# Optimization experiments

Measured on AMD Instinct MI355X. Metric: run time of the kernel, lower is better.

## Reference

```python
import jax, jax.numpy as jnp
import numpy as np

NH = 12
LEVEL = 4  # Lmin = 2**LEVEL = 16


def _build_sets(T, Lmin):
    l_list, r_list = [], []
    L = Lmin
    while L <= T:
        for i in range(T // L):
            l_list.append(i * L)
            r_list.append((i + 1) * L - 1)
        L *= 2
    return np.asarray(l_list, np.int32), np.asarray(r_list, np.int32)


def _get_slice(x_cum, l_idx, r_idx):
    # x_cum: [B,nh,T,hs]; returns inclusive range-sums x[l..r] via cumsum diffs
    r = x_cum[:, :, r_idx, :]
    l = x_cum[:, :, np.maximum(np.asarray(l_idx) - 1, 0), :]
    mask = (np.asarray(l_idx) >= 1).astype(x_cum.dtype)[None, None, :, None]
    return r - l * mask


def _get_slice_dyn(x_cum, l_idx, r_idx):
    # same but with traced/jnp indices (tail term)
    r = x_cum[:, :, r_idx, :]
    l = x_cum[:, :, jnp.maximum(l_idx - 1, 0), :]
    mask = (l_idx >= 1).astype(x_cum.dtype)[None, None, :, None]
    return r - l * mask


def setup_inputs() -> dict:
    key = jax.random.key(0)
    k0, k1, k2, k3 = jax.random.split(key, 4)
    B, T, C = 8, 2048, 768
    hs = C // NH
    s = 0.02
    return {
        "x": jax.random.normal(k0, (B, T, C), jnp.float32),
        "Wqkv": jax.random.normal(k1, (3 * C, C), jnp.float32) * s,
        "Wproj": jax.random.normal(k2, (C, C), jnp.float32) * s,
        "Wv": jax.random.normal(k3, (hs, hs * hs), jnp.float32) * s,
        "bv": jnp.zeros((hs,), jnp.float32),
    }


def reference(x, Wqkv, Wproj, Wv, bv):
    B, T, C = x.shape
    nh = NH
    hs = C // nh
    Lmin = 2 ** LEVEL
    scale = 1.0 / jnp.sqrt(jnp.asarray(hs, x.dtype))

    qkv = x @ Wqkv.T  # [B,T,3C]
    q, k, v0 = jnp.split(qkv, 3, axis=-1)
    q = q.reshape(B, T, nh, hs).transpose(0, 2, 1, 3)   # [B,nh,T,hs]
    k = k.reshape(B, T, nh, hs).transpose(0, 2, 1, 3)
    v0 = v0.reshape(B, T, nh, hs).transpose(0, 2, 1, 3)

    # v = v_proj(outer(k, v0).flatten)  == einsum with Wv reshaped [hs,hs,hs]
    Wv3 = Wv.reshape(hs, hs, hs)
    v = jnp.einsum('bhti,bhtj,eij->bhte', k, v0, Wv3) + bv

    k_cum = jnp.cumsum(k, axis=2)
    v_cum = jnp.cumsum(v, axis=2)

    l_idx, r_idx = _build_sets(T, Lmin)  # static dyadic sets
    K = _get_slice(k_cum, l_idx, r_idx)  # [B,nh,S,hs]
    V = _get_slice(v_cum, l_idx, r_idx)

    t_idx = jnp.arange(T)
    mask = t_idx[:, None] >= jnp.asarray(r_idx)[None, :]  # [T,S]
    logits = jnp.einsum('bhtd,bhsd->bhts', q, K) * scale
    logits = jnp.where(mask[None, None], logits, -jnp.inf)

    # tail: remainder within the current Lmin block
    l_tail = (t_idx // Lmin) * Lmin
    K_tail = _get_slice_dyn(k_cum, l_tail, t_idx)  # [B,nh,T,hs]
    V_tail = _get_slice_dyn(v_cum, l_tail, t_idx)
    tail_logits = jnp.sum(q * K_tail, axis=-1) * scale  # [B,nh,T]

    att = jax.nn.softmax(jnp.concatenate([logits, tail_logits[..., None]], axis=-1), axis=-1)
    out = jnp.einsum('bhts,bhsd->bhtd', att[..., :-1], V) + att[..., -1:] * V_tail
    out = out.transpose(0, 2, 1, 3).reshape(B, T, C)
    return out @ Wproj.T
```

## Files before the change

### kernel.cpp

```cpp
#include <hip/hip_runtime.h>


typedef float  f32x4  __attribute__((ext_vector_type(4)));
typedef _Float16 half8 __attribute__((ext_vector_type(8)));
typedef _Float16 half4 __attribute__((ext_vector_type(4)));

#define DEV __device__ __forceinline__
#define MFMA16(a, b, c) __builtin_amdgcn_mfma_f32_16x16x32_f16((a), (b), (c), 0, 0, 0)
#define GLOAD16(gp, lp)                                                  \
  __builtin_amdgcn_global_load_lds(                                      \
      (const __attribute__((address_space(1))) unsigned int*)(gp),       \
      (__attribute__((address_space(3))) unsigned int*)(lp), 16, 0, 0)

__global__ __launch_bounds__(256) void k_cast16(const float* __restrict__ in,
                                                _Float16* __restrict__ outh, int n4) {
  int i = blockIdx.x * 256 + threadIdx.x;
  if (i >= n4) return;
  f32x4 v = ((const f32x4*)in)[i];
  half4 o;
#pragma unroll
  for (int c = 0; c < 4; ++c) o[c] = (_Float16)v[c];
  ((half4*)outh)[i] = o;
}

__global__ __launch_bounds__(256, 3) void k_gemm_qkv(
    const _Float16* __restrict__ A16, const _Float16* __restrict__ B16,
    _Float16* __restrict__ qo, _Float16* __restrict__ ko, _Float16* __restrict__ v0o) {
  __shared__ _Float16 sA[128][64], sB[128][64];
  const int K = 768;
  int tid = threadIdx.x, lane = tid & 63, wave = tid >> 6;
  int l15 = lane & 15, g = lane >> 4;
  int wr = wave >> 1, wc = wave & 1;
  int n0 = blockIdx.x * 128, m0 = blockIdx.y * 128;
  f32x4 acc[4][4];
#pragma unroll
  for (int a = 0; a < 4; ++a)
#pragma unroll
    for (int b = 0; b < 4; ++b) acc[a][b] = f32x4{0.f, 0.f, 0.f, 0.f};
  int rsel = lane >> 3;
  int csel = (lane & 7) ^ rsel;
  for (int k0 = 0; k0 < K; k0 += 64) {
#pragma unroll
    for (int r = 0; r < 4; ++r) {
      int row = wave * 32 + r * 8 + rsel;
      GLOAD16(&A16[(size_t)(m0 + row) * K + k0 + csel * 8], &sA[wave * 32 + r * 8][0]);
      GLOAD16(&B16[(size_t)(n0 + row) * K + k0 + csel * 8], &sB[wave * 32 + r * 8][0]);
    }
    __syncthreads();
#pragma unroll
    for (int kk = 0; kk < 2; ++kk) {
      int kc = kk * 4 + g;
      int cc = ((kc ^ (l15 & 7)) << 3);
      half8 af[4], bf[4];
#pragma unroll
      for (int mf = 0; mf < 4; ++mf) af[mf] = *(const half8*)&sA[wr * 64 + mf * 16 + l15][cc];
#pragma unroll
      for (int nf = 0; nf < 4; ++nf) bf[nf] = *(const half8*)&sB[wc * 64 + nf * 16 + l15][cc];
#pragma unroll
      for (int mf = 0; mf < 4; ++mf)
#pragma unroll
        for (int nf = 0; nf < 4; ++nf)
          acc[mf][nf] = MFMA16(af[mf], bf[nf], acc[mf][nf]);
    }
    __syncthreads();
  }
  int sec = n0 / 768;
  int nb = n0 - sec * 768;
#pragma unroll
  for (int mf = 0; mf < 4; ++mf)
#pragma unroll
    for (int nf = 0; nf < 4; ++nf)
#pragma unroll
      for (int r = 0; r < 4; ++r) {
        int m = m0 + wr * 64 + mf * 16 + (g << 2) + r;
        int n = nb + wc * 64 + nf * 16 + l15;
        int b = m >> 11, t = m & 2047;
        int h = n >> 6, d = n & 63;
        size_t idx = (((size_t)b * 12 + h) * 2048 + t) * 64 + d;
        _Float16 val = (_Float16)acc[mf][nf][r];
        if (sec == 0) qo[idx] = val;
        else if (sec == 1) ko[idx] = val;
        else v0o[idx] = val;
      }
}

__global__ __launch_bounds__(256, 3) void k_veins(
    const _Float16* __restrict__ kh, const _Float16* __restrict__ v0g,
    const _Float16* __restrict__ Wvh, const float* __restrict__ bv,
    _Float16* __restrict__ vout) {
  __shared__ _Float16 ks[256][72];
  __shared__ _Float16 sB[2][64][64];
  int tid = threadIdx.x, lane = tid & 63, wave = tid >> 6;
  int l15 = lane & 15, g = lane >> 4, g8 = g << 3;
  size_t row0 = (size_t)blockIdx.x * 256;

  int srow_lo = wave * 8 + (lane >> 3);
  int scsrc = (lane & 7) ^ (lane >> 3);
  auto STAGE = [&](int b, int i) {
#pragma unroll
    for (int h = 0; h < 2; ++h) {
      GLOAD16(&Wvh[(size_t)(h * 32 + srow_lo) * 4096 + i * 64 + (scsrc << 3)],
              ((_Float16*)sB) + (size_t)b * 4096 + (h * 256 + wave * 64) * 8);
    }
  };

#pragma unroll
  for (int r = 0; r < 8; ++r) {
    int row = (tid >> 3) + r * 32;
    int c8 = (tid & 7) << 3;
    *(half8*)&ks[row][c8] = *(const half8*)&kh[(row0 + row) * 64 + c8];
  }
  half8 v0r[4][2];
#pragma unroll
  for (int mf = 0; mf < 4; ++mf) {
    size_t rb = (row0 + wave * 64 + mf * 16 + l15) * 64;
#pragma unroll
    for (int kk = 0; kk < 2; ++kk)
      v0r[mf][kk] = *(const half8*)&v0g[rb + kk * 32 + g8];
  }
  f32x4 acc[4][4];
#pragma unroll
  for (int a = 0; a < 4; ++a)
#pragma unroll
    for (int b = 0; b < 4; ++b) acc[a][b] = f32x4{0.f, 0.f, 0.f, 0.f};

  STAGE(0, 0);
  __syncthreads();
  int r0 = wave * 64 + l15;
  for (int i8 = 0; i8 < 8; ++i8) {
    half8 kr0 = *(const half8*)&ks[r0][i8 * 8];
    half8 kr1 = *(const half8*)&ks[r0 + 16][i8 * 8];
    half8 kr2 = *(const half8*)&ks[r0 + 32][i8 * 8];
    half8 kr3 = *(const half8*)&ks[r0 + 48][i8 * 8];
#pragma unroll
    for (int ii = 0; ii < 8; ++ii) {
      int i = i8 * 8 + ii;
      int cur = i & 1;
      if (i < 63) STAGE(cur ^ 1, i + 1);
      half8 b0[4], b1[4];
#pragma unroll
      for (int nf = 0; nf < 4; ++nf) {
        b0[nf] = *(const half8*)&sB[cur][nf * 16 + l15][((g ^ (l15 & 7)) << 3)];
        b1[nf] = *(const half8*)&sB[cur][nf * 16 + l15][(((4 + g) ^ (l15 & 7)) << 3)];
      }
      _Float16 kv0 = kr0[ii], kv1 = kr1[ii], kv2 = kr2[ii], kv3 = kr3[ii];
      {
        half8 a0 = v0r[0][0] * kv0, a1 = v0r[1][0] * kv1;
        half8 a2 = v0r[2][0] * kv2, a3 = v0r[3][0] * kv3;
#pragma unroll
        for (int nf = 0; nf < 4; ++nf) {
          acc[0][nf] = MFMA16(a0, b0[nf], acc[0][nf]);
          acc[1][nf] = MFMA16(a1, b0[nf], acc[1][nf]);
          acc[2][nf] = MFMA16(a2, b0[nf], acc[2][nf]);
          acc[3][nf] = MFMA16(a3, b0[nf], acc[3][nf]);
        }
      }
      {
        half8 a0 = v0r[0][1] * kv0, a1 = v0r[1][1] * kv1;
        half8 a2 = v0r[2][1] * kv2, a3 = v0r[3][1] * kv3;
#pragma unroll
        for (int nf = 0; nf < 4; ++nf) {
          acc[0][nf] = MFMA16(a0, b1[nf], acc[0][nf]);
          acc[1][nf] = MFMA16(a1, b1[nf], acc[1][nf]);
          acc[2][nf] = MFMA16(a2, b1[nf], acc[2][nf]);
          acc[3][nf] = MFMA16(a3, b1[nf], acc[3][nf]);
        }
      }
      __syncthreads();
    }
  }
#pragma unroll
  for (int mf = 0; mf < 4; ++mf)
#pragma unroll
    for (int nf = 0; nf < 4; ++nf) {
      int e = (nf << 4) + l15;
      float bve = bv[e];
#pragma unroll
      for (int r = 0; r < 4; ++r) {
        int row = wave * 64 + mf * 16 + (g << 2) + r;
        vout[(row0 + row) * 64 + e] = (_Float16)(acc[mf][nf][r] + bve);
      }
    }
}

__global__ __launch_bounds__(256) void k_segments(
    const _Float16* __restrict__ kmat, const _Float16* __restrict__ vmat,
    _Float16* __restrict__ Ks, _Float16* __restrict__ Vt) {
  __shared__ float Ls[255][64];
  int bh = blockIdx.x, tid = threadIdx.x;
  size_t bh2048 = (size_t)bh * 2048;
  for (int task = tid; task < 8192; task += 256) {
    int seg = task >> 6, d = task & 63;
    const _Float16* p = kmat + (bh2048 + seg * 16) * 64 + d;
    float s = 0.f;
#pragma unroll
    for (int u = 0; u < 16; ++u) s += (float)p[u * 64];
    Ls[seg][d] = s;
  }
  __syncthreads();
  {
    int bprev = 0, bcur = 128, cnt = 64;
    for (int lev = 1; lev < 8; ++lev) {
      for (int task = tid; task < cnt * 64; task += 256) {
        int i = task >> 6, d = task & 63;
        Ls[bcur + i][d] = Ls[bprev + 2 * i][d] + Ls[bprev + 2 * i + 1][d];
      }
      __syncthreads();
      bprev = bcur; bcur += cnt; cnt >>= 1;
    }
  }
  for (int task = tid; task < 16384; task += 256) {
    int seg = task >> 6;
    float v = (seg < 255) ? Ls[seg][task & 63] : 0.f;
    Ks[(size_t)bh * 16384 + task] = (_Float16)v;
  }
  __syncthreads();
  for (int task = tid; task < 8192; task += 256) {
    int seg = task >> 6, d = task & 63;
    const _Float16* p = vmat + (bh2048 + seg * 16) * 64 + d;
    float s = 0.f;
#pragma unroll
    for (int u = 0; u < 16; ++u) s += (float)p[u * 64];
    Ls[seg][d] = s;
  }
  __syncthreads();
  {
    int bprev = 0, bcur = 128, cnt = 64;
    for (int lev = 1; lev < 8; ++lev) {
      for (int task = tid; task < cnt * 64; task += 256) {
        int i = task >> 6, d = task & 63;
        Ls[bcur + i][d] = Ls[bprev + 2 * i][d] + Ls[bprev + 2 * i + 1][d];
      }
      __syncthreads();
      bprev = bcur; bcur += cnt; cnt >>= 1;
    }
  }
  for (int task = tid; task < 16384; task += 256) {
    int d = task >> 8, seg = task & 255;
    float v = (seg < 255) ? Ls[seg][d] : 0.f;
    Vt[(size_t)bh * 16384 + task] = (_Float16)v;
  }
}

__global__ __launch_bounds__(256) void k_attn2(
    const _Float16* __restrict__ qm, const _Float16* __restrict__ km,
    const _Float16* __restrict__ vm,
    const _Float16* __restrict__ Ks, const _Float16* __restrict__ Vt,
    _Float16* __restrict__ outp) {
  __shared__ __align__(16) _Float16 P[4][16][296];
  __shared__ __align__(16) _Float16 tK[4][16][72];
  __shared__ __align__(16) _Float16 tV[4][16][72];
  int tid = threadIdx.x, lane = tid & 63, wave = tid >> 6;
  int orig = blockIdx.y * 32 + blockIdx.x;
  int wg = (orig & 7) * 384 + (orig >> 3);
  int tile = wg & 31, bh = wg >> 5;
  int t0 = tile * 64, tw0 = t0 + wave * 16;
  size_t bh2048 = (size_t)bh * 2048;
  int l15 = lane & 15, g = lane >> 4, g8 = g << 3;

  {
    const _Float16* kp = km + (bh2048 + tw0) * 64 + lane;
    const _Float16* vp = vm + (bh2048 + tw0) * 64 + lane;
    float ka = 0.f, va = 0.f;
#pragma unroll
    for (int t = 0; t < 16; ++t) {
      ka += (float)kp[t * 64];
      va += (float)vp[t * 64];
      tK[wave][t][lane] = (_Float16)ka;
      tV[wave][t][lane] = (_Float16)va;
    }
  }
  half8 qf[2];
  {
    const _Float16* qp = qm + (bh2048 + tw0 + l15) * 64 + g8;
    qf[0] = *(const half8*)qp;
    qf[1] = *(const half8*)(qp + 32);
  }
  unsigned mA = 0, mE = 0;
#pragma unroll
  for (int nf = 0; nf < 16; ++nf) {
    int seg = nf * 16 + l15;
    if (seg < 255) {
      int m = 256 - seg;
      int cl = 32 - __clz(m - 1);
      int lev = 8 - cl;
      int rdx = (seg - (256 - (256 >> lev)) + 1) * (16 << lev) - 1;
      if (rdx < tw0) mA |= 1u << nf;
      else if (rdx == tw0 + 15) mE |= 1u << nf;
    }
  }
  unsigned mAny = mA | mE;
  unsigned pmask = 0;
#pragma unroll
  for (int ks = 0; ks < 8; ++ks)
    if (__any((int)((mAny >> (2 * ks)) & 3u))) pmask |= 1u << ks;

  f32x4 acc[17];
#pragma unroll
  for (int i = 0; i < 17; ++i) acc[i] = f32x4{0.f, 0.f, 0.f, 0.f};
  const _Float16* KsB = Ks + (size_t)bh * 16384;
#pragma unroll
  for (int ks = 0; ks < 8; ++ks) {
    if ((pmask >> ks) & 1) {
      const _Float16* ph = KsB + (size_t)(ks * 32 + l15) * 64 + g8;
      half8 h00 = *(const half8*)ph;
      half8 h01 = *(const half8*)(ph + 32);
      half8 h10 = *(const half8*)(ph + 1024);
      half8 h11 = *(const half8*)(ph + 1056);
      acc[2 * ks] = MFMA16(qf[0], h00, acc[2 * ks]);
      acc[2 * ks] = MFMA16(qf[1], h01, acc[2 * ks]);
      acc[2 * ks + 1] = MFMA16(qf[0], h10, acc[2 * ks + 1]);
      acc[2 * ks + 1] = MFMA16(qf[1], h11, acc[2 * ks + 1]);
    }
  }
  {
    const _Float16* tp = &tK[wave][l15][g8];
    half8 t0f = *(const half8*)tp;
    half8 t1f = *(const half8*)(tp + 32);
    acc[16] = MFMA16(qf[0], t0f, acc[16]);
    acc[16] = MFMA16(qf[1], t1f, acc[16]);
  }

  const float scale = 0.125f;
  float mx[4], sm[4], et[4];
#pragma unroll
  for (int r = 0; r < 4; ++r) {
    int tr = g * 4 + r;
    mx[r] = (l15 == tr) ? acc[16][r] * scale : -3.0e38f;
  }
#pragma unroll
  for (int nf = 0; nf < 16; ++nf) {
    bool bA = (mA >> nf) & 1, bE = (mE >> nf) & 1;
#pragma unroll
    for (int r = 0; r < 4; ++r) {
      bool u = bA || (bE && g == 3 && r == 3);
      if (u) mx[r] = fmaxf(mx[r], acc[nf][r] * scale);
    }
  }
#pragma unroll
  for (int off = 1; off < 16; off <<= 1)
#pragma unroll
    for (int r = 0; r < 4; ++r) mx[r] = fmaxf(mx[r], __shfl_xor(mx[r], off));
#pragma unroll
  for (int r = 0; r < 4; ++r) {
    int tr = g * 4 + r;
    et[r] = (l15 == tr) ? __expf(acc[16][r] * scale - mx[r]) : 0.f;
    sm[r] = et[r];
  }
#pragma unroll
  for (int ks = 0; ks < 8; ++ks) {
    if ((pmask >> ks) & 1) {
#pragma unroll
      for (int f = 0; f < 2; ++f) {
        int nf = 2 * ks + f;
        bool bA = (mA >> nf) & 1, bE = (mE >> nf) & 1;
#pragma unroll
        for (int r = 0; r < 4; ++r) {
          bool u = bA || (bE && g == 3 && r == 3);
          float e = u ? __expf(acc[nf][r] * scale - mx[r]) : 0.f;
          acc[nf][r] = e;
          sm[r] += e;
        }
      }
    }
  }
#pragma unroll
  for (int off = 1; off < 16; off <<= 1)
#pragma unroll
    for (int r = 0; r < 4; ++r) sm[r] += __shfl_xor(sm[r], off);
  float inv[4];
#pragma unroll
  for (int r = 0; r < 4; ++r) inv[r] = 1.f / sm[r];

  half8 zz = {};
  *(half8*)&P[wave][lane >> 2][256 + (lane & 3) * 8] = zz;
#pragma unroll
  for (int nf = 0; nf < 16; ++nf)
#pragma unroll
    for (int r = 0; r < 4; ++r)
      P[wave][g * 4 + r][nf * 16 + l15] = (_Float16)(acc[nf][r] * inv[r]);
#pragma unroll
  for (int r = 0; r < 4; ++r)
    if (l15 == g * 4 + r) P[wave][l15][256 + l15] = (_Float16)(et[r] * inv[r]);

  f32x4 oa[4];
#pragma unroll
  for (int i = 0; i < 4; ++i) oa[i] = f32x4{0.f, 0.f, 0.f, 0.f};
  const _Float16* VB = Vt + (size_t)bh * 16384;
#pragma unroll
  for (int ks = 0; ks < 8; ++ks) {
    if ((pmask >> ks) & 1) {
      half8 pa = *(const half8*)&P[wave][l15][ks * 32 + g8];
#pragma unroll
      for (int n2 = 0; n2 < 4; ++n2) {
        half8 vb = *(const half8*)(VB + (size_t)(n2 * 16 + l15) * 256 + ks * 32 + g8);
        oa[n2] = MFMA16(pa, vb, oa[n2]);
      }
    }
  }
  {
    half8 pa = *(const half8*)&P[wave][l15][256 + g8];
    int jb = (g & 1) * 8;
#pragma unroll
    for (int n2 = 0; n2 < 4; ++n2) {
      half8 vt;
#pragma unroll
      for (int jj = 0; jj < 8; ++jj) vt[jj] = tV[wave][jb + jj][n2 * 16 + l15];
      oa[n2] = MFMA16(pa, vt, oa[n2]);
    }
  }
  int b = bh / 12, h = bh - b * 12;
  size_t obase = ((size_t)b * 2048 + tw0) * 768 + h * 64;
#pragma unroll
  for (int n2 = 0; n2 < 4; ++n2)
#pragma unroll
    for (int r = 0; r < 4; ++r)
      outp[obase + (size_t)(g * 4 + r) * 768 + n2 * 16 + l15] = (_Float16)oa[n2][r];
}

__global__ __launch_bounds__(256, 3) void k_gemm_proj(
    const _Float16* __restrict__ A16, const _Float16* __restrict__ B16,
    float* __restrict__ C) {
  __shared__ _Float16 sA[128][64], sB[128][64];
  const int K = 768;
  int tid = threadIdx.x, lane = tid & 63, wave = tid >> 6;
  int l15 = lane & 15, g = lane >> 4;
  int wr = wave >> 1, wc = wave & 1;
  int n0 = blockIdx.x * 128, m0 = blockIdx.y * 128;
  f32x4 acc[4][4];
#pragma unroll
  for (int a = 0; a < 4; ++a)
#pragma unroll
    for (int b = 0; b < 4; ++b) acc[a][b] = f32x4{0.f, 0.f, 0.f, 0.f};
  int rsel = lane >> 3;
  int csel = (lane & 7) ^ rsel;
  for (int k0 = 0; k0 < K; k0 += 64) {
#pragma unroll
    for (int r = 0; r < 4; ++r) {
      int row = wave * 32 + r * 8 + rsel;
      GLOAD16(&A16[(size_t)(m0 + row) * K + k0 + csel * 8], &sA[wave * 32 + r * 8][0]);
      GLOAD16(&B16[(size_t)(n0 + row) * K + k0 + csel * 8], &sB[wave * 32 + r * 8][0]);
    }
    __syncthreads();
#pragma unroll
    for (int kk = 0; kk < 2; ++kk) {
      int kc = kk * 4 + g;
      int cc = ((kc ^ (l15 & 7)) << 3);
      half8 af[4], bf[4];
#pragma unroll
      for (int mf = 0; mf < 4; ++mf) af[mf] = *(const half8*)&sA[wr * 64 + mf * 16 + l15][cc];
#pragma unroll
      for (int nf = 0; nf < 4; ++nf) bf[nf] = *(const half8*)&sB[wc * 64 + nf * 16 + l15][cc];
#pragma unroll
      for (int mf = 0; mf < 4; ++mf)
#pragma unroll
        for (int nf = 0; nf < 4; ++nf)
          acc[mf][nf] = MFMA16(af[mf], bf[nf], acc[mf][nf]);
    }
    __syncthreads();
  }
#pragma unroll
  for (int mf = 0; mf < 4; ++mf)
#pragma unroll
    for (int nf = 0; nf < 4; ++nf)
#pragma unroll
      for (int r = 0; r < 4; ++r) {
        int m = m0 + wr * 64 + mf * 16 + (g << 2) + r;
        int n = n0 + wc * 64 + nf * 16 + l15;
        C[(size_t)m * 768 + n] = acc[mf][nf][r];
      }
}

extern "C" void kernel_launch(void* const* d_in, const int* in_sizes, int n_in,
                              void* d_out, int out_size, void* d_ws, size_t ws_size,
                              hipStream_t stream) {
  const float* x = (const float*)d_in[0];
  const float* Wqkv = (const float*)d_in[1];
  const float* Wproj = (const float*)d_in[2];
  const float* Wv = (const float*)d_in[3];
  const float* bv = (const float*)d_in[4];
  float* out = (float*)d_out;
  char* ws = (char*)d_ws;
  size_t off = 0;
  auto alloc = [&](size_t bytes) -> void* {
    void* p = (void*)(ws + off);
    off += (bytes + 255) & ~(size_t)255;
    return p;
  };
  _Float16* x16  = (_Float16*)alloc(12582912ull * 2);
  _Float16* wq16 = (_Float16*)alloc(1769472ull * 2);
  _Float16* wv16 = (_Float16*)alloc(262144ull * 2 + 8192);
  _Float16* wp16 = (_Float16*)alloc(589824ull * 2);
  _Float16* q16  = (_Float16*)alloc(12582912ull * 2);
  _Float16* k16  = (_Float16*)alloc(12582912ull * 2);
  _Float16* v016 = (_Float16*)alloc(12582912ull * 2);
  _Float16* vm16 = (_Float16*)alloc(12582912ull * 2);
  _Float16* Ks   = (_Float16*)alloc(1572864ull * 2);
  _Float16* Vt   = (_Float16*)alloc(1572864ull * 2);
  _Float16* outp = (_Float16*)alloc(12582912ull * 2);

  k_cast16<<<dim3(12288), dim3(256), 0, stream>>>(x, x16, 3145728);
  k_cast16<<<dim3(1728), dim3(256), 0, stream>>>(Wqkv, wq16, 442368);
  k_cast16<<<dim3(256), dim3(256), 0, stream>>>(Wv, wv16, 65536);
  k_cast16<<<dim3(576), dim3(256), 0, stream>>>(Wproj, wp16, 147456);
  k_gemm_qkv<<<dim3(18, 128), dim3(256), 0, stream>>>(x16, wq16, q16, k16, v016);
  k_veins<<<dim3(768), dim3(256), 0, stream>>>(k16, v016, wv16, bv, vm16);
  k_segments<<<dim3(96), dim3(256), 0, stream>>>(k16, vm16, Ks, Vt);
  k_attn2<<<dim3(32, 96), dim3(256), 0, stream>>>(q16, k16, vm16, Ks, Vt, outp);
  k_gemm_proj<<<dim3(6, 128), dim3(256), 0, stream>>>(outp, wp16, out);
}
```

Baseline: 356.2 us.

## Remap GEMM workgroups per XCD, use exp2 softmax, shrink P tile, add setprio

The QKV and projection GEMMs now launch as flat 1D grids and remap block ids so that consecutive tiles land on the same XCD, aiming for better L2 reuse of the weight and activation panels. In the attention kernel the softmax folds log2(e) into the scale and uses exp2f, and the P buffer is narrowed now that the tail block only needs 16 columns. The tail V fragment is zero-filled for the unused lane groups. s_setprio brackets the MFMA phases so waves issuing matrix work get scheduling priority. Each piece is small, and together they touch several kernels with separate tuning intents.

```diff
diff --git a/kernel.cpp b/kernel.cpp
--- a/kernel.cpp
+++ b/kernel.cpp
@@ -31,7 +31,8 @@
   int tid = threadIdx.x, lane = tid & 63, wave = tid >> 6;
   int l15 = lane & 15, g = lane >> 4;
   int wr = wave >> 1, wc = wave & 1;
-  int n0 = blockIdx.x * 128, m0 = blockIdx.y * 128;
+  int wg = (blockIdx.x & 7) * 288 + (blockIdx.x >> 3);
+  int n0 = (wg % 18) * 128, m0 = (wg / 18) * 128;
   f32x4 acc[4][4];
 #pragma unroll
   for (int a = 0; a < 4; ++a)
@@ -247,7 +248,7 @@
     const _Float16* __restrict__ vm,
     const _Float16* __restrict__ Ks, const _Float16* __restrict__ Vt,
     _Float16* __restrict__ outp) {
-  __shared__ __align__(16) _Float16 P[4][16][296];
+  __shared__ __align__(16) _Float16 P[4][16][280];
   __shared__ __align__(16) _Float16 tK[4][16][72];
   __shared__ __align__(16) _Float16 tV[4][16][72];
   int tid = threadIdx.x, lane = tid & 63, wave = tid >> 6;
@@ -299,6 +300,7 @@
 #pragma unroll
   for (int i = 0; i < 17; ++i) acc[i] = f32x4{0.f, 0.f, 0.f, 0.f};
   const _Float16* KsB = Ks + (size_t)bh * 16384;
+  __builtin_amdgcn_s_setprio(1);
 #pragma unroll
   for (int ks = 0; ks < 8; ++ks) {
     if ((pmask >> ks) & 1) {
@@ -320,13 +322,14 @@
     acc[16] = MFMA16(qf[0], t0f, acc[16]);
     acc[16] = MFMA16(qf[1], t1f, acc[16]);
   }
-
-  const float scale = 0.125f;
+  __builtin_amdgcn_s_setprio(0);
+
+  const float c = 0.125f * 1.44269504f;
   float mx[4], sm[4], et[4];
 #pragma unroll
   for (int r = 0; r < 4; ++r) {
     int tr = g * 4 + r;
-    mx[r] = (l15 == tr) ? acc[16][r] * scale : -3.0e38f;
+    mx[r] = (l15 == tr) ? acc[16][r] * c : -3.0e38f;
   }
 #pragma unroll
   for (int nf = 0; nf < 16; ++nf) {
@@ -334,7 +337,7 @@
 #pragma unroll
     for (int r = 0; r < 4; ++r) {
       bool u = bA || (bE && g == 3 && r == 3);
-      if (u) mx[r] = fmaxf(mx[r], acc[nf][r] * scale);
+      if (u) mx[r] = fmaxf(mx[r], acc[nf][r] * c);
     }
   }
 #pragma unroll
@@ -344,7 +347,7 @@
 #pragma unroll
   for (int r = 0; r < 4; ++r) {
     int tr = g * 4 + r;
-    et[r] = (l15 == tr) ? __expf(acc[16][r] * scale - mx[r]) : 0.f;
+    et[r] = (l15 == tr) ? exp2f(acc[16][r] * c - mx[r]) : 0.f;
     sm[r] = et[r];
   }
 #pragma unroll
@@ -357,7 +360,7 @@
 #pragma unroll
         for (int r = 0; r < 4; ++r) {
           bool u = bA || (bE && g == 3 && r == 3);
-          float e = u ? __expf(acc[nf][r] * scale - mx[r]) : 0.f;
+          float e = u ? exp2f(acc[nf][r] * c - mx[r]) : 0.f;
           acc[nf][r] = e;
           sm[r] += e;
         }
@@ -372,8 +375,10 @@
 #pragma unroll
   for (int r = 0; r < 4; ++r) inv[r] = 1.f / sm[r];
 
-  half8 zz = {};
-  *(half8*)&P[wave][lane >> 2][256 + (lane & 3) * 8] = zz;
+  {
+    half4 z4 = {};
+    *(half4*)&P[wave][lane >> 2][256 + (lane & 3) * 4] = z4;
+  }
 #pragma unroll
   for (int nf = 0; nf < 16; ++nf)
 #pragma unroll
@@ -387,6 +392,7 @@
 #pragma unroll
   for (int i = 0; i < 4; ++i) oa[i] = f32x4{0.f, 0.f, 0.f, 0.f};
   const _Float16* VB = Vt + (size_t)bh * 16384;
+  __builtin_amdgcn_s_setprio(1);
 #pragma unroll
   for (int ks = 0; ks < 8; ++ks) {
     if ((pmask >> ks) & 1) {
@@ -399,16 +405,18 @@
     }
   }
   {
-    half8 pa = *(const half8*)&P[wave][l15][256 + g8];
-    int jb = (g & 1) * 8;
+    half8 pa = *(const half8*)&P[wave][l15][256 + (g & 1) * 8];
 #pragma unroll
     for (int n2 = 0; n2 < 4; ++n2) {
-      half8 vt;
-#pragma unroll
-      for (int jj = 0; jj < 8; ++jj) vt[jj] = tV[wave][jb + jj][n2 * 16 + l15];
+      half8 vt = {};
+      if (g < 2) {
+#pragma unroll
+        for (int jj = 0; jj < 8; ++jj) vt[jj] = tV[wave][g8 + jj][n2 * 16 + l15];
+      }
       oa[n2] = MFMA16(pa, vt, oa[n2]);
     }
   }
+  __builtin_amdgcn_s_setprio(0);
   int b = bh / 12, h = bh - b * 12;
   size_t obase = ((size_t)b * 2048 + tw0) * 768 + h * 64;
 #pragma unroll
@@ -426,7 +434,8 @@
   int tid = threadIdx.x, lane = tid & 63, wave = tid >> 6;
   int l15 = lane & 15, g = lane >> 4;
   int wr = wave >> 1, wc = wave & 1;
-  int n0 = blockIdx.x * 128, m0 = blockIdx.y * 128;
+  int wg = (blockIdx.x & 7) * 96 + (blockIdx.x >> 3);
+  int n0 = (wg % 6) * 128, m0 = (wg / 6) * 128;
   f32x4 acc[4][4];
 #pragma unroll
   for (int a = 0; a < 4; ++a)
@@ -503,9 +512,9 @@
   k_cast16<<<dim3(1728), dim3(256), 0, stream>>>(Wqkv, wq16, 442368);
   k_cast16<<<dim3(256), dim3(256), 0, stream>>>(Wv, wv16, 65536);
   k_cast16<<<dim3(576), dim3(256), 0, stream>>>(Wproj, wp16, 147456);
-  k_gemm_qkv<<<dim3(18, 128), dim3(256), 0, stream>>>(x16, wq16, q16, k16, v016);
+  k_gemm_qkv<<<dim3(2304), dim3(256), 0, stream>>>(x16, wq16, q16, k16, v016);
   k_veins<<<dim3(768), dim3(256), 0, stream>>>(k16, v016, wv16, bv, vm16);
   k_segments<<<dim3(96), dim3(256), 0, stream>>>(k16, vm16, Ks, Vt);
   k_attn2<<<dim3(32, 96), dim3(256), 0, stream>>>(q16, k16, vm16, Ks, Vt, outp);
-  k_gemm_proj<<<dim3(6, 128), dim3(256), 0, stream>>>(outp, wp16, out);
-}
+  k_gemm_proj<<<dim3(768), dim3(256), 0, stream>>>(outp, wp16, out);
+}
```

Result: faster. 340.4 us (-4.4%).
